# Optimization experiments

Hardware: AMD Instinct MI355X
Metric: run time of the kernel (lower is better)

The kernel has to match this reference:

```python
import jax, jax.numpy as jnp
import numpy as np

NUM_HEADS = 16
NUM_KV_HEADS = 4
FEATURES = 2048
HEAD_DIM = 128
SOFT_CAP = 50.0
WINDOW = 1024
B, T = 2, 2048


def apply_rope(inputs, positions, head_dim, max_wavelength=10000):
    # inputs: [B, T, N, H], positions: [B, T]
    fraction = 2 * jnp.arange(0, head_dim // 2) / head_dim
    timescale = max_wavelength ** fraction  # [H/2]
    sinusoid = positions[..., jnp.newaxis] / timescale[jnp.newaxis, jnp.newaxis, :]  # [B,T,H/2]
    sinusoid = sinusoid[..., jnp.newaxis, :]  # [B,T,1,H/2]
    sin, cos = jnp.sin(sinusoid), jnp.cos(sinusoid)
    first, second = jnp.split(inputs, 2, axis=-1)
    out = jnp.concatenate([first * cos - second * sin, second * cos + first * sin], axis=-1)
    return out.astype(inputs.dtype)


def setup_inputs() -> dict:
    key = jax.random.key(0)
    k1, k2, k3, k4 = jax.random.split(key, 4)
    x = jax.random.normal(k1, (B, T, FEATURES), dtype=jnp.float32)
    segment_pos = jnp.tile(jnp.arange(T, dtype=jnp.int32)[None, :], (B, 1))
    attn_mask = jnp.tril(jnp.ones((T, T), dtype=bool))[None, :, :].repeat(B, axis=0)  # causal [B,T,S]
    std = 0.02
    wq = jax.random.normal(k2, (NUM_HEADS, FEATURES, HEAD_DIM), dtype=jnp.float32) * std
    wkv = jax.random.normal(k3, (2, NUM_KV_HEADS, FEATURES, HEAD_DIM), dtype=jnp.float32) * std
    wvec = jax.random.normal(k4, (NUM_HEADS, HEAD_DIM, FEATURES), dtype=jnp.float32) * std
    return {"x": x, "segment_pos": segment_pos, "attn_mask": attn_mask, "wq": wq, "wkv": wkv, "wvec": wvec}


def reference(x, segment_pos, attn_mask, wq, wkv, wvec):
    # projections
    q = jnp.einsum('BTD,NDH->BTNH', x, wq)                 # [B,T,N,H]
    k, v = jnp.einsum('BSD,CKDH->CBSKH', x, wkv)           # each [B,S,K,H]
    # RoPE + scale
    q = apply_rope(q, segment_pos, HEAD_DIM)
    q = q * jnp.reciprocal(jnp.sqrt(jnp.float32(HEAD_DIM))).astype(q.dtype)
    k = apply_rope(k, segment_pos, HEAD_DIM)
    # GQA logits
    b, t, n, h = q.shape
    g = n // NUM_KV_HEADS
    qg = q.reshape(b, t, NUM_KV_HEADS, g, h)
    logits = jnp.einsum('BTKGH,BSKH->BTKGS', qg, k).reshape(b, t, n, -1)  # [B,T,N,S]
    # soft cap
    logits = jnp.tanh(logits / SOFT_CAP) * SOFT_CAP
    # sliding-window mask combined with causal mask
    ones = jnp.ones_like(attn_mask)
    sliding = jnp.triu(ones, -WINDOW + 1) * jnp.tril(ones, WINDOW - 1)
    mask = sliding * attn_mask  # [B,T,S]
    padded = jnp.where(mask[:, :, None, :], logits, jnp.finfo(logits.dtype).min)
    probs = jax.nn.softmax(padded, axis=-1).astype(k.dtype)
    # GQA weighted values
    pg = probs.reshape(b, t, NUM_KV_HEADS, g, -1)
    enc = jnp.einsum('BTKGS,BSKH->BTKGH', pg, v).reshape(b, t, n, h)
    out = jnp.einsum('BTNH,NHD->BTD', enc, wvec)
    return out
```

## Files before the change

### kernel.cpp

```cpp
#include <hip/hip_runtime.h>
#include <hip/hip_bf16.h>

#define DEVINL static __device__ __forceinline__

typedef __attribute__((ext_vector_type(4))) float f32x4;
typedef __attribute__((ext_vector_type(8))) short bf16x8;

DEVINL short f2bf(float f) {
  __hip_bfloat16 h = __float2bfloat16(f);
  union { __hip_bfloat16 h; short s; } u; u.h = h; return u.s;
}
DEVINL float bf2f(short s) {
  union { unsigned u; float f; } v; v.u = ((unsigned)(unsigned short)s) << 16;
  return v.f;
}
DEVINL float ldf(float x) { return x; }
DEVINL float ldf(short x) { return bf2f(x); }

__global__ void k_cvt(const float* __restrict__ in, short* __restrict__ out, int n4) {
  int i = blockIdx.x * blockDim.x + threadIdx.x;
  if (i >= n4) return;
  const float4 v = reinterpret_cast<const float4*>(in)[i];
  short4 o;
  o.x = f2bf(v.x); o.y = f2bf(v.y); o.z = f2bf(v.z); o.w = f2bf(v.w);
  reinterpret_cast<short4*>(out)[i] = o;
}

template <typename Tin>
__global__ void k_tr(const Tin* __restrict__ in, short* __restrict__ out, int R, int C) {
  __shared__ float tile[32][33];
  const int bz = blockIdx.z;
  const int r0 = blockIdx.y * 32, c0 = blockIdx.x * 32;
  const int tx = threadIdx.x & 31, ty = threadIdx.x >> 5;
  const Tin* ip = in + (size_t)bz * R * C;
  short* op = out + (size_t)bz * R * C;
#pragma unroll
  for (int k = 0; k < 4; k++)
    tile[ty + k * 8][tx] = ldf(ip[(size_t)(r0 + ty + k * 8) * C + c0 + tx]);
  __syncthreads();
#pragma unroll
  for (int k = 0; k < 4; k++)
    op[(size_t)(c0 + ty + k * 8) * R + r0 + tx] = f2bf(tile[tx][ty + k * 8]);
}


#define GBAR __builtin_amdgcn_s_barrier()
#define LGK asm volatile("s_waitcnt lgkmcnt(0)")
#define PR1 __builtin_amdgcn_s_setprio(1)
#define PR0 __builtin_amdgcn_s_setprio(0)
#define VMW { if constexpr (LPA + LPB == 4) asm volatile("s_waitcnt vmcnt(4)"); \
              else asm volatile("s_waitcnt vmcnt(3)"); }

template <int LN>
DEVINL void stage(char* dst, const short* src, int K, int tid) {
#pragma unroll
  for (int L = 0; L < LN; L++) {
    const int loc = L * 8192 + tid * 16;
    const int row = loc >> 7;
    const int gsw = ((loc >> 4) & 7) ^ (row & 7);
    __builtin_amdgcn_global_load_lds(
        (const __attribute__((address_space(1))) void*)(src + (size_t)row * K + gsw * 8),
        (__attribute__((address_space(3))) void*)(dst + loc), 16, 0, 0);
  }
}

#define SA(BUF, HALF, KT) \
  stage<LPA>((BUF) + (HALF) * (ABY / 2), Am + (size_t)((HALF) * (BM / 2)) * K + (KT) * 64, K, tid)
#define SB(BUF, HALF, KT) \
  stage<LPB>((BUF) + (HALF) * (BBY / 2), Bn + (size_t)((HALF) * (BN / 2)) * K + (KT) * 64, K, tid)

#define RDA(BUF, IH)                                                                   \
  { _Pragma("unroll")                                                                  \
    for (int kf_ = 0; kf_ < KFN; kf_++) {                                              \
      _Pragma("unroll")                                                                \
      for (int kk_ = 0; kk_ < 2; kk_++) {                                              \
        const int row_ = ((IH) * KFN + kf_) * 32 + wr * 16 + lr;                       \
        a[kf_ * 2 + kk_] = *(const bf16x8*)((BUF) + row_ * 128 +                       \
                                            (((kk_ * 4 + lu) ^ (lr & 7)) << 4));       \
      } } }

#define RDB(BUF, JH, ARR)                                                              \
  { _Pragma("unroll")                                                                  \
    for (int jf_ = 0; jf_ < JFN; jf_++) {                                              \
      _Pragma("unroll")                                                                \
      for (int kk_ = 0; kk_ < 2; kk_++) {                                              \
        const int row_ = ((JH) * JFN + jf_) * 64 + wc * 16 + lr;                       \
        ARR[jf_ * 2 + kk_] = *(const bf16x8*)((BUF) + row_ * 128 +                     \
                                              (((kk_ * 4 + lu) ^ (lr & 7)) << 4));     \
      } } }

#define MF(IH, JH, ARR)                                                                \
  { _Pragma("unroll")                                                                  \
    for (int kf_ = 0; kf_ < KFN; kf_++)                                                \
      { _Pragma("unroll")                                                              \
        for (int jf_ = 0; jf_ < JFN; jf_++)                                            \
          { _Pragma("unroll")                                                          \
            for (int kk_ = 0; kk_ < 2; kk_++)                                          \
              acc[(IH) * KFN + kf_][(JH) * JFN + jf_] =                                \
                  __builtin_amdgcn_mfma_f32_16x16x32_bf16(                             \
                      a[kf_ * 2 + kk_], ARR[jf_ * 2 + kk_],                            \
                      acc[(IH) * KFN + kf_][(JH) * JFN + jf_], 0, 0, 0);               \
          } } }

template <int BM, int BN>
__global__ __launch_bounds__(512, 2) void k_gemm256(
    const short* __restrict__ A, const short* __restrict__ Bt,
    void* __restrict__ Out0, void* __restrict__ Out1,
    int N, int K, int mode) {
  constexpr int LPA = BM / 128;
  constexpr int LPB = BN / 128;
  constexpr int KFN = BM / 64;
  constexpr int JFN = BN / 128;
  constexpr int ABY = BM * 128;
  constexpr int BBY = BN * 128;
  extern __shared__ __align__(16) char sm[];
  char* A0 = sm;
  char* A1 = sm + ABY;
  char* B0 = sm + 2 * ABY;
  char* B1 = sm + 2 * ABY + BBY;
  const int lin = blockIdx.x + gridDim.x * blockIdx.y;
  const int m0 = (lin >> 3) * BM, n0 = (lin & 7) * BN;
  const int tid = threadIdx.x, lane = tid & 63, w = tid >> 6;
  const int wr = w & 1, wc = w >> 1;
  const int lr = lane & 15, lu = lane >> 4;
  const short* Am = A + (size_t)m0 * K;
  const short* Bn = Bt + (size_t)n0 * K;
  f32x4 acc[KFN * 2][JFN * 2] = {};
  bf16x8 a[KFN * 2], bJ0[JFN * 2], bJ1[JFN * 2];
  const int NIT = K >> 7;
  const int TMAX = (K >> 6) - 1;

  SA(A0, 0, 0); SB(B0, 1, 0); SA(A0, 1, 0); SB(B0, 0, 0);
  SA(A1, 0, 1); SB(B1, 1, 1);
  VMW; GBAR;

  for (int it = 0; it < NIT; ++it) {
    const int t1 = 2 * it + 1;
    const int t2 = (2 * it + 2 < TMAX) ? 2 * it + 2 : TMAX;
    const int t3 = (2 * it + 3 < TMAX) ? 2 * it + 3 : TMAX;
    RDA(A0, 0); RDB(B0, 0, bJ0); RDB(B0, 1, bJ1); SA(A1, 1, t1); SB(B1, 0, t1);
    GBAR; LGK; PR1; MF(0, 0, bJ0); MF(0, 1, bJ1); PR0; GBAR;
    RDA(A0, 1); SA(A0, 0, t2); SB(B0, 1, t2);
    GBAR; LGK; PR1; MF(1, 1, bJ1); MF(1, 0, bJ0); PR0; VMW; GBAR;
    RDA(A1, 0); RDB(B1, 0, bJ0); RDB(B1, 1, bJ1); SA(A0, 1, t2); SB(B0, 0, t2);
    GBAR; LGK; PR1; MF(0, 0, bJ0); MF(0, 1, bJ1); PR0; GBAR;
    RDA(A1, 1); SA(A1, 0, t3); SB(B1, 1, t3);
    GBAR; LGK; PR1; MF(1, 1, bJ1); MF(1, 0, bJ0); PR0; VMW; GBAR;
  }

  if (mode == 2) {
#pragma unroll
    for (int k = 0; k < KFN * 2; k++)
#pragma unroll
      for (int j = 0; j < JFN * 2; j++)
#pragma unroll
        for (int r = 0; r < 4; r++) {
          const int m = m0 + k * 32 + wr * 16 + lu * 4 + r;
          const int n = n0 + j * 64 + wc * 16 + lr;
          ((float*)Out0)[(size_t)m * N + n] = acc[k][j][r];
        }
  } else {
    const int i_rope = wc * 16 + lr;
    const float inv = __expf(-(float)i_rope * (float)(9.210340371976184 / 64.0));
#pragma unroll
    for (int k = 0; k < KFN * 2; k++) {
      float sn[4], cs[4];
#pragma unroll
      for (int r = 0; r < 4; r++) {
        const int m = m0 + k * 32 + wr * 16 + lu * 4 + r;
        sincosf((float)(m & 2047) * inv, &sn[r], &cs[r]);
      }
#pragma unroll
      for (int u = 0; u < JFN; u++) {
        const int n_lo = n0 + (2 * u) * 64 + wc * 16 + lr;
        const int reg = (n_lo < 2048) ? 0 : ((n_lo < 2560) ? 1 : 2);
#pragma unroll
        for (int r = 0; r < 4; r++) {
          const int m = m0 + k * 32 + wr * 16 + lu * 4 + r;
          const int bb = m >> 11, t = m & 2047;
          float lo = acc[k][2 * u][r], hi = acc[k][2 * u + 1][r];
          if (reg < 2) {
            const float l2 = lo * cs[r] - hi * sn[r];
            const float h2 = hi * cs[r] + lo * sn[r];
            const float sc = (reg == 0) ? 0.08838834764831845f : 1.0f;
            lo = l2 * sc; hi = h2 * sc;
          }
#pragma unroll
          for (int p = 0; p < 2; p++) {
            const int n = n_lo + p * 64;
            const float v = p ? hi : lo;
            if (n < 2048) {
              ((short*)Out0)[(((size_t)(bb * 16 + (n >> 7))) << 18) + t * 128 + (n & 127)] =
                  f2bf(v);
            } else {
              const int nn = n - 2048;
              ((short*)Out1)[(((size_t)(((nn >> 9) * 2 + bb) * 4 + ((nn >> 7) & 3))) << 18) +
                             t * 128 + (nn & 127)] = f2bf(v);
            }
          }
        }
      }
    }
  }
}

__global__ __launch_bounds__(256) void k_attn(
    const short* __restrict__ q, const short* __restrict__ kk,
    const short* __restrict__ vT, short* __restrict__ enc) {
  __shared__ __align__(16) short lK[64 * 128];
  __shared__ __align__(16) short lV[128 * 64];
  __shared__ __align__(16) short lP[4][16 * 64];
  const int bn = blockIdx.x, b = bn >> 4, n = bn & 15, kv = n >> 2;
  const int qt0 = (31 - blockIdx.y) * 64;
  const int tid = threadIdx.x, lane = tid & 63, w = tid >> 6;
  const int lr = lane & 15, lu = lane >> 4;
  const short* qbase = q + (((size_t)(b * 16 + n)) << 18) + (size_t)(qt0 + w * 16) * 128;
  bf16x8 qa[4];
#pragma unroll
  for (int c = 0; c < 4; c++)
    qa[c] = *reinterpret_cast<const bf16x8*>(qbase + lr * 128 + c * 32 + lu * 8);
  f32x4 o[8] = {};
  float lsum = 0.f;
  const short* kbase = kk + (((size_t)(b * 4 + kv)) << 18);
  const short* vbase = vT + (((size_t)(b * 4 + kv)) << 18);
  char* lPw = (char*)lP[w];
  const int tw = qt0 + w * 16;
  const int t_row = tw + lu * 4;
  int st0 = qt0 - 1023; if (st0 < 0) st0 = 0;
  st0 >>= 6;
  const int stE = (qt0 + 63) >> 6;
  for (int st = st0; st <= stE; st++) {
    const int s0 = st << 6;
#pragma unroll
    for (int c = 0; c < 4; c++) {
      const int L = w * 4096 + c * 1024 + lane * 16;
      {
        const int s = L >> 8, slot = (L >> 4) & 15;
        const int sp = slot ^ (s & 7);
        __builtin_amdgcn_global_load_lds(
            (const __attribute__((address_space(1))) void*)(kbase + (size_t)(s0 + s) * 128 + sp * 8),
            (__attribute__((address_space(3))) void*)((char*)lK + L), 16, 0, 0);
      }
      {
        const int h = L >> 7, slot = (L >> 4) & 7;
        const int u = slot ^ (h & 7);
        __builtin_amdgcn_global_load_lds(
            (const __attribute__((address_space(1))) void*)(vbase + (size_t)h * 2048 + s0 + u * 8),
            (__attribute__((address_space(3))) void*)((char*)lV + L), 16, 0, 0);
      }
    }
    __syncthreads();
    f32x4 sc[4];
    __builtin_amdgcn_s_setprio(1);
#pragma unroll
    for (int cg = 0; cg < 4; cg++) {
      sc[cg] = (f32x4){0.f, 0.f, 0.f, 0.f};
      const int s = cg * 16 + lr;
      const int sw = (s & 7) << 4;
#pragma unroll
      for (int c = 0; c < 4; c++) {
        bf16x8 kb = *reinterpret_cast<const bf16x8*>((char*)lK + s * 256 + (((c * 4 + lu) << 4) ^ sw));
        sc[cg] = __builtin_amdgcn_mfma_f32_16x16x32_bf16(kb, qa[c], sc[cg], 0, 0, 0);
      }
    }
    __builtin_amdgcn_s_setprio(0);
    const bool allv = (s0 + 63 <= tw) && (s0 + 1008 >= tw);
    if (allv) {
#pragma unroll
      for (int cg = 0; cg < 4; cg++) {
        float pr[4];
#pragma unroll
        for (int r = 0; r < 4; r++) {
          const float x = sc[cg][r];
          const float cap = __builtin_fmaf(x * x * x, -1.3333333e-4f, x);
          const float p = __expf(cap);
          lsum += p;
          pr[r] = p;
        }
        unsigned w0, w1;
        asm("v_cvt_pk_bf16_f32 %0, %1, %2" : "=v"(w0) : "v"(pr[0]), "v"(pr[1]));
        asm("v_cvt_pk_bf16_f32 %0, %1, %2" : "=v"(w1) : "v"(pr[2]), "v"(pr[3]));
        const int sb = (cg * 16 + lu * 4) << 1;
        *(unsigned*)(lPw + (lr << 7) + (sb ^ ((lr & 7) << 4))) = w0;
        *(unsigned*)(lPw + (lr << 7) + ((sb + 4) ^ ((lr & 7) << 4))) = w1;
      }
    } else {
      const int t = tw + lr;
#pragma unroll
      for (int cg = 0; cg < 4; cg++) {
        float pr[4];
#pragma unroll
        for (int r = 0; r < 4; r++) {
          const int s = s0 + cg * 16 + lu * 4 + r;
          const bool valid = (s <= t) & (s + 1024 > t);
          const float x = sc[cg][r];
          const float cap = __builtin_fmaf(x * x * x, -1.3333333e-4f, x);
          float p = __expf(cap);
          p = valid ? p : 0.f;
          lsum += p;
          pr[r] = p;
        }
        unsigned w0, w1;
        asm("v_cvt_pk_bf16_f32 %0, %1, %2" : "=v"(w0) : "v"(pr[0]), "v"(pr[1]));
        asm("v_cvt_pk_bf16_f32 %0, %1, %2" : "=v"(w1) : "v"(pr[2]), "v"(pr[3]));
        const int sb = (cg * 16 + lu * 4) << 1;
        *(unsigned*)(lPw + (lr << 7) + (sb ^ ((lr & 7) << 4))) = w0;
        *(unsigned*)(lPw + (lr << 7) + ((sb + 4) ^ ((lr & 7) << 4))) = w1;
      }
    }
#pragma unroll
    for (int ks = 0; ks < 2; ks++) {
      const bf16x8 pf = *reinterpret_cast<const bf16x8*>(
          lPw + (lr << 7) + ((ks * 64 + lu * 16) ^ ((lr & 7) << 4)));
      __builtin_amdgcn_s_setprio(1);
#pragma unroll
      for (int oc = 0; oc < 8; oc++) {
        const int h = oc * 16 + lr;
        bf16x8 vb = *reinterpret_cast<const bf16x8*>(
            (char*)lV + h * 128 + (((ks * 4 + lu) << 4) ^ ((h & 7) << 4)));
        o[oc] = __builtin_amdgcn_mfma_f32_16x16x32_bf16(pf, vb, o[oc], 0, 0, 0);
      }
      __builtin_amdgcn_s_setprio(0);
    }
    __syncthreads();
  }
  float tot = lsum;
  tot += __shfl_xor(tot, 16, 64);
  tot += __shfl_xor(tot, 32, 64);
  float rs[4];
#pragma unroll
  for (int r = 0; r < 4; r++)
    rs[r] = 1.f / __shfl(tot, lu * 4 + r, 64);
#pragma unroll
  for (int oc = 0; oc < 8; oc++)
#pragma unroll
    for (int r = 0; r < 4; r++) {
      const int t = t_row + r;
      enc[((size_t)b * 2048 + t) * 2048 + n * 128 + oc * 16 + lr] = f2bf(o[oc][r] * rs[r]);
    }
}

extern "C" void kernel_launch(void* const* d_in, const int* in_sizes, int n_in,
                              void* d_out, int out_size, void* d_ws, size_t ws_size,
                              hipStream_t stream) {
  (void)in_sizes; (void)n_in; (void)out_size; (void)ws_size;
  const float* x    = (const float*)d_in[0];
  const float* wq   = (const float*)d_in[3];
  const float* wkv  = (const float*)d_in[4];
  const float* wvec = (const float*)d_in[5];
  char* ws = (char*)d_ws;
  size_t off = 0;
  short* xbf   = (short*)(ws + off); off += (size_t)8388608 * 2;
  short* wall  = (short*)(ws + off); off += (size_t)3072 * 2048 * 2;
  short* wvecT = (short*)(ws + off); off += (size_t)2048 * 2048 * 2;
  short* qbuf  = (short*)(ws + off); off += (size_t)2 * 16 * 2048 * 128 * 2;
  short* kvbuf = (short*)(ws + off); off += (size_t)2 * 2 * 4 * 2048 * 128 * 2;
  short* vTbuf = (short*)(ws + off); off += (size_t)2 * 4 * 128 * 2048 * 2;
  short* encb  = (short*)(ws + off); off += (size_t)2 * 2048 * 2048 * 2;

  hipFuncSetAttribute(reinterpret_cast<const void*>(&k_gemm256<128, 384>),
                      hipFuncAttributeMaxDynamicSharedMemorySize, 131072);
  hipFuncSetAttribute(reinterpret_cast<const void*>(&k_gemm256<128, 256>),
                      hipFuncAttributeMaxDynamicSharedMemorySize, 98304);

  k_cvt<<<8192, 256, 0, stream>>>(x, xbf, 2097152);
  k_tr<float><<<dim3(4, 64, 16), 256, 0, stream>>>(wq, wall, 2048, 128);
  k_tr<float><<<dim3(4, 64, 4), 256, 0, stream>>>(wkv, wall + 4194304, 2048, 128);
  k_tr<float><<<dim3(4, 64, 4), 256, 0, stream>>>(wkv + 1048576, wall + 5242880, 2048, 128);
  k_tr<float><<<dim3(64, 64, 1), 256, 0, stream>>>(wvec, wvecT, 2048, 2048);
  k_gemm256<128, 384><<<dim3(32, 8), 512, 131072, stream>>>(xbf, wall, qbuf, kvbuf,
                                                            3072, 2048, 0);
  k_tr<short><<<dim3(4, 64, 8), 256, 0, stream>>>(kvbuf + 2097152, vTbuf, 2048, 128);
  k_attn<<<dim3(32, 32), 256, 0, stream>>>(qbuf, kvbuf, vTbuf, encb);
  k_gemm256<128, 256><<<dim3(32, 8), 512, 98304, stream>>>(encb, wvecT, d_out, nullptr,
                                                           2048, 2048, 2);
}
```

Baseline: 173.0 us.

## Add dedicated 256x256-tile QKV GEMM with permuted weight rows for RoPE pairing

Replaces the generic 128x384-tile QKV projection GEMM with a specialized 256x256-tile kernel that uses an 8-phase double-buffered pipeline. The Q and K weight columns are permuted during transposition so each wave holds both RoPE halves in its own accumulators. The output GEMM is reduced to a single plain store path. The larger square tile is meant to raise arithmetic intensity and reuse, at the cost of fewer blocks (192) and a more complex, layout-dependent epilogue.

Result: slower. 211.6 us (+22.3%).

```diff
diff --git a/kernel.cpp b/kernel.cpp
--- a/kernel.cpp
+++ b/kernel.cpp
@@ -26,7 +26,7 @@
   reinterpret_cast<short4*>(out)[i] = o;
 }
 
-template <typename Tin>
+template <typename Tin, bool PERM>
 __global__ void k_tr(const Tin* __restrict__ in, short* __restrict__ out, int R, int C) {
   __shared__ float tile[32][33];
   const int bz = blockIdx.z;
@@ -39,17 +39,21 @@
     tile[ty + k * 8][tx] = ldf(ip[(size_t)(r0 + ty + k * 8) * C + c0 + tx]);
   __syncthreads();
 #pragma unroll
-  for (int k = 0; k < 4; k++)
-    op[(size_t)(c0 + ty + k * 8) * R + r0 + tx] = f2bf(tile[tx][ty + k * 8]);
-}
-
+  for (int k = 0; k < 4; k++) {
+    const int cc = c0 + ty + k * 8;
+    int p = cc;
+    if (PERM) {
+      const int hi = cc >> 6, g = cc & 63;
+      p = ((g >> 4) & 1) * 64 + ((g >> 5) * 2 + hi) * 16 + (g & 15);
+    }
+    op[(size_t)p * R + r0 + tx] = f2bf(tile[tx][ty + k * 8]);
+  }
+}
 
 #define GBAR __builtin_amdgcn_s_barrier()
 #define LGK asm volatile("s_waitcnt lgkmcnt(0)")
 #define PR1 __builtin_amdgcn_s_setprio(1)
 #define PR0 __builtin_amdgcn_s_setprio(0)
-#define VMW { if constexpr (LPA + LPB == 4) asm volatile("s_waitcnt vmcnt(4)"); \
-              else asm volatile("s_waitcnt vmcnt(3)"); }
 
 template <int LN>
 DEVINL void stage(char* dst, const short* src, int K, int tid) {
@@ -63,6 +67,140 @@
         (__attribute__((address_space(3))) void*)(dst + loc), 16, 0, 0);
   }
 }
+
+
+#define QRDA(BUF, HALF)                                                                \
+  { _Pragma("unroll")                                                                  \
+    for (int kf_ = 0; kf_ < 4; kf_++) {                                                \
+      _Pragma("unroll")                                                                \
+      for (int kk_ = 0; kk_ < 2; kk_++) {                                              \
+        const int row_ = wr * 128 + ((HALF) * 4 + kf_) * 16 + lr;                      \
+        a[kf_ * 2 + kk_] = *(const bf16x8*)((BUF) + row_ * 128 +                       \
+                                            (((kk_ * 4 + lu) ^ (lr & 7)) << 4));       \
+      } } }
+
+#define QRDB(BUF, HALF)                                                                \
+  { _Pragma("unroll")                                                                  \
+    for (int jf_ = 0; jf_ < 2; jf_++) {                                                \
+      _Pragma("unroll")                                                                \
+      for (int kk_ = 0; kk_ < 2; kk_++) {                                              \
+        const int row_ = wc * 64 + ((HALF) * 2 + jf_) * 16 + lr;                       \
+        b[jf_ * 2 + kk_] = *(const bf16x8*)((BUF) + row_ * 128 +                       \
+                                            (((kk_ * 4 + lu) ^ (lr & 7)) << 4));       \
+      } } }
+
+#define QMF(FO, JO)                                                                    \
+  { _Pragma("unroll")                                                                  \
+    for (int kf_ = 0; kf_ < 4; kf_++)                                                  \
+      { _Pragma("unroll")                                                              \
+        for (int jf_ = 0; jf_ < 2; jf_++)                                              \
+          { _Pragma("unroll")                                                          \
+            for (int kk_ = 0; kk_ < 2; kk_++)                                          \
+              acc[(FO) * 4 + kf_][(JO) * 2 + jf_] =                                    \
+                  __builtin_amdgcn_mfma_f32_16x16x32_bf16(                             \
+                      a[kf_ * 2 + kk_], b[jf_ * 2 + kk_],                              \
+                      acc[(FO) * 4 + kf_][(JO) * 2 + jf_], 0, 0, 0);                   \
+          } } }
+
+#define SAH(BUF, H, T) stage<2>((BUF) + (H) * 16384, Am + (size_t)((H) * 128) * K + (T) * 64, K, tid)
+#define SBH(BUF, H, T) stage<2>((BUF) + (H) * 16384, Bn + (size_t)((H) * 128) * K + (T) * 64, K, tid)
+#define VM2 asm volatile("s_waitcnt vmcnt(2)")
+
+__global__ __launch_bounds__(512, 2) void k_gqkv(
+    const short* __restrict__ A, const short* __restrict__ Bt,
+    void* __restrict__ Out0, void* __restrict__ Out1, int K) {
+  extern __shared__ __align__(16) char sm[];
+  char* A0 = sm;
+  char* A1 = sm + 32768;
+  char* B0 = sm + 65536;
+  char* B1 = sm + 98304;
+  const int m0 = blockIdx.x * 256, n0 = blockIdx.y * 256;
+  const int tid = threadIdx.x, lane = tid & 63, w = tid >> 6;
+  const int wr = w >> 2, wc = w & 3;
+  const int lr = lane & 15, lu = lane >> 4;
+  const short* Am = A + (size_t)m0 * K;
+  const short* Bn = Bt + (size_t)n0 * K;
+  f32x4 acc[8][4] = {};
+  bf16x8 a[8], b[4];
+  const int NIT = K >> 7, TMAX = (K >> 6) - 1;
+
+  SAH(A0, 0, 0); SAH(A0, 1, 0); SBH(B0, 0, 0); SBH(B0, 1, 0);
+  SAH(A1, 0, 1);
+  VM2; GBAR;
+
+  for (int it = 0; it < NIT; ++it) {
+    const int o = 2 * it + 1;
+    const int e2 = (2 * it + 2 < TMAX) ? 2 * it + 2 : TMAX;
+    const int o2 = (2 * it + 3 < TMAX) ? 2 * it + 3 : TMAX;
+    QRDA(A0, 0); QRDB(B0, 0); SAH(A1, 1, o);
+    GBAR; LGK; PR1; QMF(0, 0); PR0; GBAR;
+    QRDB(B0, 1); SBH(B1, 0, o);
+    GBAR; LGK; PR1; QMF(0, 1); PR0; GBAR;
+    QRDA(A0, 1); SBH(B1, 1, o);
+    GBAR; LGK; PR1; QMF(1, 1); PR0; GBAR;
+    QRDB(B0, 0); SAH(A0, 0, e2);
+    GBAR; LGK; PR1; QMF(1, 0); PR0; VM2; GBAR;
+    QRDA(A1, 0); QRDB(B1, 0); SAH(A0, 1, e2);
+    GBAR; LGK; PR1; QMF(0, 0); PR0; GBAR;
+    QRDB(B1, 1); SBH(B0, 0, e2);
+    GBAR; LGK; PR1; QMF(0, 1); PR0; GBAR;
+    QRDA(A1, 1); SBH(B0, 1, e2);
+    GBAR; LGK; PR1; QMF(1, 1); PR0; GBAR;
+    QRDB(B1, 0); SAH(A1, 0, o2);
+    GBAR; LGK; PR1; QMF(1, 0); PR0; VM2; GBAR;
+  }
+
+  const bool isq = (n0 < 2048);
+  const bool isv = (n0 >= 2560);
+  const int wcH = wc & 1;
+  const float g0f = (float)(wcH * 16 + lr);
+  const float inv0 = __expf(-g0f * (float)(9.210340371976184 / 64.0));
+  const float inv1 = __expf(-(g0f + 32.f) * (float)(9.210340371976184 / 64.0));
+  const int n_hb = n0 + (wc >> 1) * 128;
+#pragma unroll
+  for (int f = 0; f < 8; f++) {
+#pragma unroll
+    for (int r = 0; r < 4; r++) {
+      const int m = m0 + wr * 128 + f * 16 + lu * 4 + r;
+      const int bb = m >> 11, t = m & 2047;
+#pragma unroll
+      for (int u = 0; u < 2; u++) {
+        float lo = acc[f][2 * u][r], hi = acc[f][2 * u + 1][r];
+        if (!isv) {
+          float sn, cs;
+          sincosf((float)t * (u ? inv1 : inv0), &sn, &cs);
+          const float l2 = lo * cs - hi * sn;
+          const float h2 = hi * cs + lo * sn;
+          const float scq = isq ? 0.08838834764831845f : 1.0f;
+          lo = l2 * scq; hi = h2 * scq;
+          const int g = 32 * u + 16 * wcH + lr;
+          if (isq) {
+            short* q0 = (short*)Out0 + (((size_t)(bb * 16 + (n_hb >> 7))) << 18) +
+                        (size_t)t * 128;
+            q0[g] = f2bf(lo); q0[g + 64] = f2bf(hi);
+          } else {
+            const int nnb = n_hb - 2048;
+            short* k0 = (short*)Out1 +
+                        (((size_t)(((nnb >> 9) * 2 + bb) * 4 + ((nnb >> 7) & 3))) << 18) +
+                        (size_t)t * 128;
+            k0[g] = f2bf(lo); k0[g + 64] = f2bf(hi);
+          }
+        } else {
+#pragma unroll
+          for (int p2 = 0; p2 < 2; p2++) {
+            const int n = n0 + wc * 64 + (2 * u + p2) * 16 + lr;
+            const int nn = n - 2048;
+            ((short*)Out1)[(((size_t)(((nn >> 9) * 2 + bb) * 4 + ((nn >> 7) & 3))) << 18) +
+                           (size_t)t * 128 + (nn & 127)] = f2bf(p2 ? hi : lo);
+          }
+        }
+      }
+    }
+  }
+}
+
+#define VMW { if constexpr (LPA + LPB == 4) asm volatile("s_waitcnt vmcnt(4)"); \
+              else asm volatile("s_waitcnt vmcnt(3)"); }
 
 #define SA(BUF, HALF, KT) \
   stage<LPA>((BUF) + (HALF) * (ABY / 2), Am + (size_t)((HALF) * (BM / 2)) * K + (KT) * 64, K, tid)
@@ -105,8 +243,7 @@
 template <int BM, int BN>
 __global__ __launch_bounds__(512, 2) void k_gemm256(
     const short* __restrict__ A, const short* __restrict__ Bt,
-    void* __restrict__ Out0, void* __restrict__ Out1,
-    int N, int K, int mode) {
+    void* __restrict__ Out0, int N, int K) {
   constexpr int LPA = BM / 128;
   constexpr int LPB = BN / 128;
   constexpr int KFN = BM / 64;
@@ -148,60 +285,16 @@
     GBAR; LGK; PR1; MF(1, 1, bJ1); MF(1, 0, bJ0); PR0; VMW; GBAR;
   }
 
-  if (mode == 2) {
-#pragma unroll
-    for (int k = 0; k < KFN * 2; k++)
-#pragma unroll
-      for (int j = 0; j < JFN * 2; j++)
-#pragma unroll
-        for (int r = 0; r < 4; r++) {
-          const int m = m0 + k * 32 + wr * 16 + lu * 4 + r;
-          const int n = n0 + j * 64 + wc * 16 + lr;
-          ((float*)Out0)[(size_t)m * N + n] = acc[k][j][r];
-        }
-  } else {
-    const int i_rope = wc * 16 + lr;
-    const float inv = __expf(-(float)i_rope * (float)(9.210340371976184 / 64.0));
-#pragma unroll
-    for (int k = 0; k < KFN * 2; k++) {
-      float sn[4], cs[4];
+#pragma unroll
+  for (int k = 0; k < KFN * 2; k++)
+#pragma unroll
+    for (int j = 0; j < JFN * 2; j++)
 #pragma unroll
       for (int r = 0; r < 4; r++) {
         const int m = m0 + k * 32 + wr * 16 + lu * 4 + r;
-        sincosf((float)(m & 2047) * inv, &sn[r], &cs[r]);
-      }
-#pragma unroll
-      for (int u = 0; u < JFN; u++) {
-        const int n_lo = n0 + (2 * u) * 64 + wc * 16 + lr;
-        const int reg = (n_lo < 2048) ? 0 : ((n_lo < 2560) ? 1 : 2);
-#pragma unroll
-        for (int r = 0; r < 4; r++) {
-          const int m = m0 + k * 32 + wr * 16 + lu * 4 + r;
-          const int bb = m >> 11, t = m & 2047;
-          float lo = acc[k][2 * u][r], hi = acc[k][2 * u + 1][r];
-          if (reg < 2) {
-            const float l2 = lo * cs[r] - hi * sn[r];
-            const float h2 = hi * cs[r] + lo * sn[r];
-            const float sc = (reg == 0) ? 0.08838834764831845f : 1.0f;
-            lo = l2 * sc; hi = h2 * sc;
-          }
-#pragma unroll
-          for (int p = 0; p < 2; p++) {
-            const int n = n_lo + p * 64;
-            const float v = p ? hi : lo;
-            if (n < 2048) {
-              ((short*)Out0)[(((size_t)(bb * 16 + (n >> 7))) << 18) + t * 128 + (n & 127)] =
-                  f2bf(v);
-            } else {
-              const int nn = n - 2048;
-              ((short*)Out1)[(((size_t)(((nn >> 9) * 2 + bb) * 4 + ((nn >> 7) & 3))) << 18) +
-                             t * 128 + (nn & 127)] = f2bf(v);
-            }
-          }
-        }
-      }
-    }
-  }
+        const int n = n0 + j * 64 + wc * 16 + lr;
+        ((float*)Out0)[(size_t)m * N + n] = acc[k][j][r];
+      }
 }
 
 __global__ __launch_bounds__(256) void k_attn(
@@ -358,20 +451,18 @@
   short* vTbuf = (short*)(ws + off); off += (size_t)2 * 4 * 128 * 2048 * 2;
   short* encb  = (short*)(ws + off); off += (size_t)2 * 2048 * 2048 * 2;
 
-  hipFuncSetAttribute(reinterpret_cast<const void*>(&k_gemm256<128, 384>),
+  hipFuncSetAttribute(reinterpret_cast<const void*>(&k_gqkv),
                       hipFuncAttributeMaxDynamicSharedMemorySize, 131072);
   hipFuncSetAttribute(reinterpret_cast<const void*>(&k_gemm256<128, 256>),
                       hipFuncAttributeMaxDynamicSharedMemorySize, 98304);
 
   k_cvt<<<8192, 256, 0, stream>>>(x, xbf, 2097152);
-  k_tr<float><<<dim3(4, 64, 16), 256, 0, stream>>>(wq, wall, 2048, 128);
-  k_tr<float><<<dim3(4, 64, 4), 256, 0, stream>>>(wkv, wall + 4194304, 2048, 128);
-  k_tr<float><<<dim3(4, 64, 4), 256, 0, stream>>>(wkv + 1048576, wall + 5242880, 2048, 128);
-  k_tr<float><<<dim3(64, 64, 1), 256, 0, stream>>>(wvec, wvecT, 2048, 2048);
-  k_gemm256<128, 384><<<dim3(32, 8), 512, 131072, stream>>>(xbf, wall, qbuf, kvbuf,
-                                                            3072, 2048, 0);
-  k_tr<short><<<dim3(4, 64, 8), 256, 0, stream>>>(kvbuf + 2097152, vTbuf, 2048, 128);
+  k_tr<float, true><<<dim3(4, 64, 16), 256, 0, stream>>>(wq, wall, 2048, 128);
+  k_tr<float, true><<<dim3(4, 64, 4), 256, 0, stream>>>(wkv, wall + 4194304, 2048, 128);
+  k_tr<float, false><<<dim3(4, 64, 4), 256, 0, stream>>>(wkv + 1048576, wall + 5242880, 2048, 128);
+  k_tr<float, false><<<dim3(64, 64, 1), 256, 0, stream>>>(wvec, wvecT, 2048, 2048);
+  k_gqkv<<<dim3(16, 12), 512, 131072, stream>>>(xbf, wall, qbuf, kvbuf, 2048);
+  k_tr<short, false><<<dim3(4, 64, 8), 256, 0, stream>>>(kvbuf + 2097152, vTbuf, 2048, 128);
   k_attn<<<dim3(32, 32), 256, 0, stream>>>(qbuf, kvbuf, vTbuf, encb);
-  k_gemm256<128, 256><<<dim3(32, 8), 512, 98304, stream>>>(encb, wvecT, d_out, nullptr,
-                                                           2048, 2048, 2);
-}
+  k_gemm256<128, 256><<<dim3(32, 8), 512, 98304, stream>>>(encb, wvecT, d_out, 2048, 2048);
+}
```
